# Kernel tuning notes

Measured on AMD Instinct MI355X. Metric: run time of the kernel, lower is better.

The kernel has to match this reference:

```python
import jax, jax.numpy as jnp
import numpy as np

D_MODEL = 768
N_HEADS = 12

def setup_inputs() -> dict:
    key = jax.random.key(0)
    ks = jax.random.split(key, 5)
    D = D_MODEL
    x = jax.random.normal(ks[0], (2, 4096, D), dtype=jnp.float32)
    s_attn = 1.0 / np.sqrt(D)
    s_proj = 1.0 / np.sqrt(D)
    W_attn = jax.random.uniform(ks[1], (D, 3 * D), minval=-s_attn, maxval=s_attn, dtype=jnp.float32)
    b_attn = jax.random.uniform(ks[2], (3 * D,), minval=-s_attn, maxval=s_attn, dtype=jnp.float32)
    W_proj = jax.random.uniform(ks[3], (D, D), minval=-s_proj, maxval=s_proj, dtype=jnp.float32)
    b_proj = jax.random.uniform(ks[4], (D,), minval=-s_proj, maxval=s_proj, dtype=jnp.float32)
    return {"x": x, "W_attn": W_attn, "b_attn": b_attn, "W_proj": W_proj, "b_proj": b_proj}

def reference(x, W_attn, b_attn, W_proj, b_proj):
    B, T, C = x.shape
    H = N_HEADS
    hd = C // H
    qkv = x @ W_attn + b_attn                     # [B,T,3C]
    q, k, v = jnp.split(qkv, 3, axis=-1)
    # [B,T,C] -> [B,H,T,hd]
    q = q.reshape(B, T, H, hd).transpose(0, 2, 1, 3)
    k = k.reshape(B, T, H, hd).transpose(0, 2, 1, 3)
    v = v.reshape(B, T, H, hd).transpose(0, 2, 1, 3)
    att = jnp.einsum('bhqd,bhkd->bhqk', q, k) * (1.0 / np.sqrt(hd))
    causal = jnp.tril(jnp.ones((T, T), dtype=bool))
    att = jnp.where(causal, att, -jnp.inf)
    att = jax.nn.softmax(att, axis=-1)
    y = jnp.einsum('bhqk,bhkd->bhqd', att, v)     # [B,H,T,hd]
    y = y.transpose(0, 2, 1, 3).reshape(B, T, C)
    return y @ W_proj + b_proj
```

## Files before the change

### kernel.cpp

```cpp
#include <hip/hip_runtime.h>
#include <hip/hip_bf16.h>

typedef __attribute__((ext_vector_type(8))) short bf16x8;
typedef __attribute__((ext_vector_type(4))) float f32x4;
typedef __attribute__((ext_vector_type(16))) float f32x16;
typedef __attribute__((ext_vector_type(4))) int i32x4;

#define DEVI __device__ __forceinline__

namespace {
constexpr int BATCH = 2;
constexpr int T = 4096;
constexpr int C = 768;
constexpr int H = 12;
constexpr int HD = 64;
constexpr int M = BATCH * T;
constexpr int N3 = 3 * C;
constexpr int BH = BATCH * H;
constexpr float QSCALE = 0.125f * 1.44269504088896f;
constexpr int PSZ = 64 * 128 + 128;
}

DEVI ushort f2b(float f) {
  union { float f; unsigned u; } v; v.f = f;
  unsigned r = (v.u + 0x7FFFu + ((v.u >> 16) & 1u)) >> 16;
  return (ushort)r;
}

DEVI f32x16 zero16() {
  f32x16 z;
#pragma unroll
  for (int i = 0; i < 16; i++) z[i] = 0.f;
  return z;
}

DEVI void gload16(const void* g, void* l) {
  __builtin_amdgcn_global_load_lds(
      (const __attribute__((address_space(1))) unsigned int*)g,
      (__attribute__((address_space(3))) unsigned int*)l, 16, 0, 0);
}

__global__ __launch_bounds__(256) void cvt_kernel(const float* __restrict__ src,
                                                  ushort* __restrict__ dst, int n) {
  int i = (blockIdx.x * 256 + threadIdx.x) * 4;
  int stride = gridDim.x * 256 * 4;
  for (; i < n; i += stride) {
    float4 v = *reinterpret_cast<const float4*>(src + i);
    ushort4 o;
    o.x = f2b(v.x); o.y = f2b(v.y); o.z = f2b(v.z); o.w = f2b(v.w);
    *reinterpret_cast<ushort4*>(dst + i) = o;
  }
}

__global__ __launch_bounds__(256) void cvtT_kernel(const float* __restrict__ src,
                                                   ushort* __restrict__ dst,
                                                   int K, int N) {
  __shared__ ushort Lt[64 * 68];
  const int k0 = blockIdx.x * 64, n0 = blockIdx.y * 64;
  const int tid = threadIdx.x;
  const int rr = tid >> 4, c4 = (tid & 15) * 4;
#pragma unroll
  for (int it = 0; it < 4; it++) {
    const int r = it * 16 + rr;
    float4 v = *reinterpret_cast<const float4*>(src + (size_t)(k0 + r) * N + n0 + c4);
    Lt[(c4 + 0) * 68 + r] = f2b(v.x);
    Lt[(c4 + 1) * 68 + r] = f2b(v.y);
    Lt[(c4 + 2) * 68 + r] = f2b(v.z);
    Lt[(c4 + 3) * 68 + r] = f2b(v.w);
  }
  __syncthreads();
#pragma unroll
  for (int it = 0; it < 4; it++) {
    const int r = it * 16 + rr;
    *reinterpret_cast<ushort4*>(dst + (size_t)(n0 + r) * K + k0 + c4) =
        *reinterpret_cast<const ushort4*>(&Lt[r * 68 + c4]);
  }
}

template <int EPI>
__global__ __launch_bounds__(256, 3) void gemm_kernel(
    const ushort* __restrict__ A, const ushort* __restrict__ Bt,
    const float* __restrict__ bias, int N, int Kd,
    ushort* __restrict__ qo, ushort* __restrict__ ko, ushort* __restrict__ vo,
    float* __restrict__ fo) {
  constexpr int BM = 128;
  constexpr int BN = 128;
  constexpr int WN = 2;
  constexpr int WTN = BN / WN;
  constexpr int NT = WTN / 32;
  constexpr int CH_A = BM / 8;
  constexpr int CH_B = BN / 8;
  constexpr int CPW = (CH_A + CH_B) / 4;
  constexpr int SMEM = (EPI == 0) ? (4 * 64 * 68) : ((BM + BN) * 64);
  __shared__ ushort smem[SMEM];
  ushort* As = smem;
  ushort* Bs = smem + BM * 64;

  const int tid = threadIdx.x;
  const int lane = tid & 63;
  const int w = tid >> 6;
  const int l31 = lane & 31;
  const int hi = lane >> 5;
  const int wm = w / WN, wn = w % WN;
  const int m0 = blockIdx.y * BM, n0 = blockIdx.x * BN;
  const int r8 = lane >> 3, c8 = lane & 7;
  const int csw = (c8 ^ r8) * 8;

  f32x16 acc[2][NT];
#pragma unroll
  for (int mt = 0; mt < 2; mt++)
#pragma unroll
    for (int nt = 0; nt < NT; nt++) acc[mt][nt] = zero16();

  for (int k0 = 0; k0 < Kd; k0 += 64) {
    __syncthreads();
#pragma unroll
    for (int ci = 0; ci < CPW; ci++) {
      const int chk = w * CPW + ci;
      if (chk < CH_A) {
        gload16(A + (size_t)(m0 + chk * 8 + r8) * Kd + k0 + csw, (char*)As + chk * 1024);
      } else {
        const int ch2 = chk - CH_A;
        gload16(Bt + (size_t)(n0 + ch2 * 8 + r8) * Kd + k0 + csw, (char*)Bs + ch2 * 1024);
      }
    }
    __syncthreads();
#pragma unroll
    for (int ks = 0; ks < 4; ks++) {
      bf16x8 af[2], bf[NT];
#pragma unroll
      for (int mt = 0; mt < 2; mt++) {
        const int rl = wm * 64 + mt * 32 + l31;
        af[mt] = *reinterpret_cast<const bf16x8*>(
            &As[rl * 64 + ((ks * 16 + hi * 8) ^ ((rl & 7) * 8))]);
      }
#pragma unroll
      for (int nt = 0; nt < NT; nt++) {
        const int nl = wn * WTN + nt * 32 + l31;
        bf[nt] = *reinterpret_cast<const bf16x8*>(
            &Bs[nl * 64 + ((ks * 16 + hi * 8) ^ ((nl & 7) * 8))]);
      }
#pragma unroll
      for (int mt = 0; mt < 2; mt++)
#pragma unroll
        for (int nt = 0; nt < NT; nt++)
          acc[mt][nt] = __builtin_amdgcn_mfma_f32_32x32x16_bf16(af[mt], bf[nt], acc[mt][nt], 0, 0, 0);
    }
  }

  if constexpr (EPI == 0) {
    if (n0 >= 1536) {
      __syncthreads();
      ushort* Vw = smem + w * 4352;
      const float bv0 = bias[n0 + wn * 64 + l31];
      const float bv1 = bias[n0 + wn * 64 + 32 + l31];
#pragma unroll
      for (int mt = 0; mt < 2; mt++)
#pragma unroll
        for (int nt = 0; nt < 2; nt++) {
          const float bv = nt ? bv1 : bv0;
#pragma unroll
          for (int r = 0; r < 16; r++) {
            const int trow = mt * 32 + (r & 3) + ((r >> 2) << 3) + (hi << 2);
            Vw[(nt * 32 + l31) * 68 + trow] = f2b(acc[mt][nt][r] + bv);
          }
        }
      const int hh = (n0 - 1536) / 64 + wn;
      const int bb = m0 >> 12;
      const int t0 = (m0 & (T - 1)) + wm * 64;
      const size_t vbase = (size_t)((bb * H + hh) * 64 + lane) * T + t0;
#pragma unroll
      for (int x8 = 0; x8 < 8; x8++) {
        bf16x8 vv = *reinterpret_cast<const bf16x8*>(&Vw[lane * 68 + x8 * 8]);
        *reinterpret_cast<bf16x8*>(vo + vbase + ((x8 ^ (lane & 7)) * 8)) = vv;
      }
    } else {
#pragma unroll
      for (int mt = 0; mt < 2; mt++)
#pragma unroll
        for (int nt = 0; nt < 2; nt++) {
          const int n = n0 + wn * 64 + nt * 32 + l31;
          const float bv = bias[n];
          const int part = (n >= 768) ? 1 : 0;
          const int ci = n - part * 768;
          const int hh = ci >> 6, dd = ci & 63;
#pragma unroll
          for (int r = 0; r < 16; r++) {
            const int m = m0 + wm * 64 + mt * 32 + (r & 3) + ((r >> 2) << 3) + (hi << 2);
            const int bb = m >> 12, t = m & (T - 1);
            const float val = acc[mt][nt][r] + bv;
            if (part == 0) {
              qo[((size_t)(bb * H + hh) * T + t) * HD + dd] = f2b(val * QSCALE);
            } else {
              ko[((size_t)(bb * H + hh) * T + t) * HD + (dd ^ ((t & 7) << 3))] = f2b(val);
            }
          }
        }
    }
  } else {
#pragma unroll
    for (int mt = 0; mt < 2; mt++)
#pragma unroll
      for (int nt = 0; nt < NT; nt++) {
        const int n = n0 + wn * WTN + nt * 32 + l31;
        const float bv = bias[n];
#pragma unroll
        for (int r = 0; r < 16; r++) {
          const int m = m0 + wm * 64 + mt * 32 + (r & 3) + ((r >> 2) << 3) + (hi << 2);
          fo[(size_t)m * N + n] = acc[mt][nt][r] + bv;
        }
      }
  }
}

__global__ __launch_bounds__(256, 3) void attn_kernel(
    const ushort* __restrict__ Qg, const ushort* __restrict__ Kg,
    const ushort* __restrict__ Vtg, ushort* __restrict__ Yg,
    float* __restrict__ Pp) {
  __shared__ ushort kbuf[128 * 64];
  __shared__ ushort vbuf[2 * 2 * 64 * 64];

  const int tid = threadIdx.x;
  const int lane = tid & 63;
  const int w = tid >> 6;
  const int l31 = lane & 31;
  const int hi = lane >> 5;
  const int r8 = lane >> 3, c8 = lane & 7;

  const int bid = blockIdx.x;
  const int xcd = bid & 7, idx = bid >> 3;
  const int bh = xcd * 3 + idx % 3;
  const int slot = idx / 3;

  int qtA, qtB, kvbase, bnd, ntot, pA, pB;
  if (slot < 8) {
    qtA = slot; qtB = 15 - slot; kvbase = 0; bnd = slot + 1; ntot = 17; pA = -1; pB = -1;
  } else if (slot < 24) {
    qtA = slot + 8; qtB = -1; kvbase = 0; bnd = 100; ntot = 16;
    pA = (bh * 16 + (qtA - 16)) * 2; pB = -1;
  } else {
    const int a = slot - 24;
    qtA = 16 + a; qtB = 31 - a; kvbase = 16; bnd = a + 1; ntot = 17;
    pA = (bh * 16 + a) * 2 + 1; pB = (bh * 16 + (15 - a)) * 2 + 1;
  }

  const int bb = bh / H, h = bh % H;
  const ushort* Qp = Qg + (size_t)bh * T * HD;
  const char* Kbp = (const char*)(Kg + (size_t)bh * T * HD);
  const char* Vbp = (const char*)(Vtg + (size_t)bh * HD * T);

  bf16x8 qcur[4];
#pragma unroll
  for (int ks = 0; ks < 4; ks++)
    qcur[ks] = *reinterpret_cast<const bf16x8*>(
        Qp + (size_t)(qtA * 128 + w * 32 + l31) * HD + ks * 16 + hi * 8);

  int q0 = qtA * 128, q0w = q0 + w * 32, qc = q0w + l31;
  int pcur = pA;

  const f32x16 ZF = zero16();
  const i32x4 onesi = {0x3F803F80, 0x3F803F80, 0x3F803F80, 0x3F803F80};
  const bf16x8 onesf = __builtin_bit_cast(bf16x8, onesi);

  f32x16 o16[2];
  o16[0] = zero16();
  o16[1] = zero16();
  f32x16 o_l = zero16();
  const int swz = (l31 & 7) << 3;

  auto issue_K = [&](int kvt) {
    const int kv0 = kvt * 128;
#pragma unroll
    for (int c2 = 0; c2 < 4; c2++) {
      const int chk = w * 4 + c2;
      gload16(Kbp + ((size_t)(kv0 + chk * 8 + r8) * 64 + c8 * 8) * 2,
              (char*)kbuf + chk * 1024);
    }
  };
  auto issue_V = [&](int kvt, int par) {
    const int kv0 = kvt * 128;
#pragma unroll
    for (int c2 = 0; c2 < 4; c2++) {
      const int chk = w * 4 + c2;
      const int st = chk >> 3;
      const int d8 = chk & 7;
      gload16(Vbp + ((size_t)(d8 * 8 + r8) * T + kv0 + st * 64 + c8 * 8) * 2,
              (char*)vbuf + par * 16384 + chk * 1024);
    }
  };

  auto epilogue = [&](int q0p, float lr, ushort* Ytb) {
    ushort* Yw = Ytb + w * 1152;
    const float linv = 1.0f / lr;
#pragma unroll
    for (int dt = 0; dt < 2; dt++) {
#pragma unroll
      for (int r = 0; r < 16; r++) {
        const int d32 = (r & 3) + ((r >> 2) << 3) + (hi << 2);
        Yw[l31 * 36 + d32] = f2b(o16[dt][r] * linv);
      }
#pragma unroll
      for (int seg = 0; seg < 2; seg++) {
        bf16x8 vv = *reinterpret_cast<const bf16x8*>(&Yw[l31 * 36 + hi * 16 + seg * 8]);
        *reinterpret_cast<bf16x8*>(
            Yg + ((size_t)(bb * T + q0p + w * 32 + l31)) * C + h * 64 + dt * 32 +
            hi * 16 + seg * 8) = vv;
      }
    }
  };

  auto pwrite = [&](float* P, float lr) {
#pragma unroll
    for (int dt = 0; dt < 2; dt++)
#pragma unroll
      for (int r = 0; r < 16; r++) {
        const int d = dt * 32 + (r & 3) + ((r >> 2) << 3) + (hi << 2);
        P[d * 128 + w * 32 + l31] = o16[dt][r];
      }
    P[8192 + w * 32 + l31] = lr;
  };

  issue_K(kvbase);
  issue_V(kvbase, 0);

  for (int tt = 0; tt < ntot; tt++) {
    asm volatile("s_waitcnt vmcnt(0)" ::: "memory");
    __builtin_amdgcn_s_barrier();
    __builtin_amdgcn_sched_barrier(0);

    if (tt == bnd) {
      const float lr = o_l[0];
      if (pcur >= 0) pwrite(Pp + (size_t)pcur * PSZ, lr);
      else epilogue(q0, lr, vbuf + ((tt + 1) & 1) * 8192);
      o16[0] = zero16(); o16[1] = zero16(); o_l = zero16();
#pragma unroll
      for (int ks = 0; ks < 4; ks++)
        qcur[ks] = *reinterpret_cast<const bf16x8*>(
            Qp + (size_t)(qtB * 128 + w * 32 + l31) * HD + ks * 16 + hi * 8);
      q0 = qtB * 128; q0w = q0 + w * 32; qc = q0w + l31; pcur = pB;
    }

    const int kvt = kvbase + (tt < bnd ? tt : tt - bnd);
    const int kv0 = kvt * 128;
    bool have[4], needm[4];
#pragma unroll
    for (int sub = 0; sub < 4; sub++) {
      have[sub] = (kv0 + sub * 32) <= (q0w + 31);
      needm[sub] = (kv0 + sub * 32 + 31) > q0w;
    }

    f32x16 s2[4];
#pragma unroll
    for (int sub = 0; sub < 4; sub++) {
      if (!have[sub]) continue;
      const int row = sub * 32 + l31;
      __builtin_amdgcn_s_setprio(1);
      bf16x8 kf = *reinterpret_cast<const bf16x8*>(&kbuf[row * 64 + ((hi * 8) ^ swz)]);
      f32x16 acc = __builtin_amdgcn_mfma_f32_32x32x16_bf16(kf, qcur[0], ZF, 0, 0, 0);
#pragma unroll
      for (int ks = 1; ks < 4; ks++) {
        kf = *reinterpret_cast<const bf16x8*>(
            &kbuf[row * 64 + ((ks * 16 + hi * 8) ^ swz)]);
        acc = __builtin_amdgcn_mfma_f32_32x32x16_bf16(kf, qcur[ks], acc, 0, 0, 0);
      }
      __builtin_amdgcn_s_setprio(0);
      if (needm[sub]) {
#pragma unroll
        for (int r2 = 0; r2 < 16; r2++) {
          const int kv = kv0 + sub * 32 + (r2 & 3) + ((r2 >> 2) << 3) + (hi << 2);
          if (kv > qc) acc[r2] = -1e30f;
        }
      }
      s2[sub] = acc;
    }

    asm volatile("s_waitcnt lgkmcnt(0)" ::: "memory");
    __builtin_amdgcn_s_barrier();
    __builtin_amdgcn_sched_barrier(0);
    if (tt + 1 < ntot) {
      const int nkvt = kvbase + ((tt + 1) < bnd ? (tt + 1) : (tt + 1) - bnd);
      issue_K(nkvt);
      issue_V(nkvt, (tt + 1) & 1);
    }

#pragma unroll
    for (int sub = 0; sub < 4; sub++) {
      if (!have[sub]) continue;
#pragma unroll
      for (int r2 = 0; r2 < 16; r2++)
        s2[sub][r2] = __builtin_amdgcn_exp2f(s2[sub][r2]);
    }

    const ushort* Vpar = vbuf + (tt & 1) * 8192;
#pragma unroll
    for (int sub = 0; sub < 4; sub++) {
      if (!have[sub]) continue;
      const ushort* Vst = Vpar + (sub >> 1) * 4096;
      const int colb = (sub & 1) * 32;
#pragma unroll
      for (int ks2 = 0; ks2 < 2; ks2++) {
        const int r0 = ks2 * 8;
        int a0, a1, b0, b1;
        asm("v_cvt_pk_bf16_f32 %0, %1, %2" : "=v"(a0) : "v"(s2[sub][r0 + 0]), "v"(s2[sub][r0 + 1]));
        asm("v_cvt_pk_bf16_f32 %0, %1, %2" : "=v"(a1) : "v"(s2[sub][r0 + 2]), "v"(s2[sub][r0 + 3]));
        asm("v_cvt_pk_bf16_f32 %0, %1, %2" : "=v"(b0) : "v"(s2[sub][r0 + 4]), "v"(s2[sub][r0 + 5]));
        asm("v_cvt_pk_bf16_f32 %0, %1, %2" : "=v"(b1) : "v"(s2[sub][r0 + 6]), "v"(s2[sub][r0 + 7]));
        asm("v_permlane32_swap_b32 %0, %1" : "+v"(a0), "+v"(b0));
        asm("v_permlane32_swap_b32 %0, %1" : "+v"(a1), "+v"(b1));
        const i32x4 pi = {a0, a1, b0, b1};
        const bf16x8 pf = __builtin_bit_cast(bf16x8, pi);
        __builtin_amdgcn_s_setprio(1);
#pragma unroll
        for (int dt = 0; dt < 2; dt++) {
          const int drow = dt * 32 + l31;
          const int sw2 = (drow & 7) << 3;
          bf16x8 vf = *reinterpret_cast<const bf16x8*>(
              &Vst[drow * 64 + ((colb + ks2 * 16 + hi * 8) ^ sw2)]);
          o16[dt] = __builtin_amdgcn_mfma_f32_32x32x16_bf16(vf, pf, o16[dt], 0, 0, 0);
        }
        o_l = __builtin_amdgcn_mfma_f32_32x32x16_bf16(onesf, pf, o_l, 0, 0, 0);
        __builtin_amdgcn_s_setprio(0);
      }
    }
  }

  {
    const float lr = o_l[0];
    if (pcur >= 0) pwrite(Pp + (size_t)pcur * PSZ, lr);
    else epilogue(q0, lr, vbuf + (ntot & 1) * 8192);
  }
}

__global__ __launch_bounds__(128) void combine_kernel(const float* __restrict__ Pp,
                                                      ushort* __restrict__ Yg) {
  __shared__ ushort Yt[128 * 68];
  const int bid = blockIdx.x;
  const int bh = bid >> 4, qq = bid & 15;
  const int bb = bh / H, h = bh % H;
  const int q0 = (16 + qq) * 128;
  const int q = threadIdx.x;
  const float* P1 = Pp + (size_t)(bh * 16 + qq) * 2 * PSZ;
  const float* P2 = P1 + PSZ;
  const float inv = 1.0f / (P1[8192 + q] + P2[8192 + q]);
#pragma unroll 8
  for (int d = 0; d < 64; d++)
    Yt[q * 68 + d] = f2b((P1[d * 128 + q] + P2[d * 128 + q]) * inv);
  __syncthreads();
#pragma unroll
  for (int it = 0; it < 2; it++) {
    const int row = it * 64 + (q >> 1), half = q & 1;
#pragma unroll
    for (int seg = 0; seg < 4; seg++) {
      bf16x8 vv = *reinterpret_cast<const bf16x8*>(&Yt[row * 68 + half * 32 + seg * 8]);
      *reinterpret_cast<bf16x8*>(
          Yg + ((size_t)(bb * T + q0 + row)) * C + h * 64 + half * 32 + seg * 8) = vv;
    }
  }
}

extern "C" void kernel_launch(void* const* d_in, const int* in_sizes, int n_in,
                              void* d_out, int out_size, void* d_ws, size_t ws_size,
                              hipStream_t stream) {
  const float* x = (const float*)d_in[0];
  const float* Wa = (const float*)d_in[1];
  const float* ba = (const float*)d_in[2];
  const float* Wp = (const float*)d_in[3];
  const float* bp = (const float*)d_in[4];
  float* out = (float*)d_out;

  char* ws = (char*)d_ws;
  size_t off = 0;
  auto carve = [&](size_t bytes) {
    void* p = ws + off;
    off += (bytes + 255) & ~(size_t)255;
    return p;
  };
  ushort* xb   = (ushort*)carve((size_t)M * C * 2);
  ushort* WaT  = (ushort*)carve((size_t)N3 * C * 2);
  ushort* WpT  = (ushort*)carve((size_t)C * C * 2);
  ushort* Qb   = (ushort*)carve((size_t)BH * T * HD * 2);
  ushort* Kb   = (ushort*)carve((size_t)BH * T * HD * 2);
  ushort* Vtb  = (ushort*)carve((size_t)BH * HD * T * 2);
  ushort* Yb   = (ushort*)carve((size_t)M * C * 2);
  float*  Pp   = (float*)carve((size_t)BH * 16 * 2 * PSZ * 4);

  cvt_kernel<<<2048, 256, 0, stream>>>(x, xb, M * C);
  cvtT_kernel<<<dim3(C / 64, N3 / 64), 256, 0, stream>>>(Wa, WaT, C, N3);
  cvtT_kernel<<<dim3(C / 64, C / 64), 256, 0, stream>>>(Wp, WpT, C, C);

  gemm_kernel<0><<<dim3(N3 / 128, M / 128), 256, 0, stream>>>(
      xb, WaT, ba, N3, C, Qb, Kb, Vtb, nullptr);

  attn_kernel<<<dim3(768), 256, 0, stream>>>(Qb, Kb, Vtb, Yb, Pp);
  combine_kernel<<<dim3(BH * 16), 128, 0, stream>>>(Pp, Yb);

  gemm_kernel<1><<<dim3(C / 128, M / 128), 256, 0, stream>>>(
      Yb, WpT, bp, C, C, nullptr, nullptr, nullptr, out);
}
```

Measured before the change: 189.0 us.

## Replace ones-MFMA row-sum with VALU accumulation and rotate KV tile order

The softmax denominator used to come from an extra MFMA against a ones matrix on every PV step. It is now built from four scalar accumulators added alongside the exp2 calls, then combined across the lane halves with a shuffle. Separately, each block now walks its KV tiles in a rotated order based on its block id, to spread concurrent K/V loads across memory. The first part removes a third of the PV-phase MFMAs at the cost of extra VALU adds. The rotation changes which tiles neighbouring blocks read at the same time, but the masked diagonal tile may now run in a different position in the loop.

```diff
diff --git a/kernel.cpp b/kernel.cpp
--- a/kernel.cpp
+++ b/kernel.cpp
@@ -244,6 +244,19 @@
     pA = (bh * 16 + a) * 2 + 1; pB = (bh * 16 + (15 - a)) * 2 + 1;
   }
 
+  const int lenA = (bnd < ntot) ? bnd : ntot;
+  const int lenB = ntot - lenA;
+  const int rotA = (lenA > 1) ? (bid % lenA) : 0;
+  const int rotB = (lenB > 1) ? (bid % lenB) : 0;
+  auto kvt_of = [&](int tt) {
+    if (tt < lenA) {
+      int i = tt + rotA; if (i >= lenA) i -= lenA;
+      return kvbase + i;
+    }
+    int i = (tt - lenA) + rotB; if (i >= lenB) i -= lenB;
+    return kvbase + i;
+  };
+
   const int bb = bh / H, h = bh % H;
   const ushort* Qp = Qg + (size_t)bh * T * HD;
   const char* Kbp = (const char*)(Kg + (size_t)bh * T * HD);
@@ -259,13 +272,11 @@
   int pcur = pA;
 
   const f32x16 ZF = zero16();
-  const i32x4 onesi = {0x3F803F80, 0x3F803F80, 0x3F803F80, 0x3F803F80};
-  const bf16x8 onesf = __builtin_bit_cast(bf16x8, onesi);
 
   f32x16 o16[2];
   o16[0] = zero16();
   o16[1] = zero16();
-  f32x16 o_l = zero16();
+  float sa = 0.f, sb = 0.f, sc = 0.f, sd = 0.f;
   const int swz = (l31 & 7) << 3;
 
   auto issue_K = [&](int kvt) {
@@ -320,8 +331,8 @@
     P[8192 + w * 32 + l31] = lr;
   };
 
-  issue_K(kvbase);
-  issue_V(kvbase, 0);
+  issue_K(kvt_of(0));
+  issue_V(kvt_of(0), 0);
 
   for (int tt = 0; tt < ntot; tt++) {
     asm volatile("s_waitcnt vmcnt(0)" ::: "memory");
@@ -329,10 +340,12 @@
     __builtin_amdgcn_sched_barrier(0);
 
     if (tt == bnd) {
-      const float lr = o_l[0];
+      float lr = (sa + sb) + (sc + sd);
+      lr += __shfl_xor(lr, 32);
       if (pcur >= 0) pwrite(Pp + (size_t)pcur * PSZ, lr);
       else epilogue(q0, lr, vbuf + ((tt + 1) & 1) * 8192);
-      o16[0] = zero16(); o16[1] = zero16(); o_l = zero16();
+      o16[0] = zero16(); o16[1] = zero16();
+      sa = sb = sc = sd = 0.f;
 #pragma unroll
       for (int ks = 0; ks < 4; ks++)
         qcur[ks] = *reinterpret_cast<const bf16x8*>(
@@ -340,7 +353,7 @@
       q0 = qtB * 128; q0w = q0 + w * 32; qc = q0w + l31; pcur = pB;
     }
 
-    const int kvt = kvbase + (tt < bnd ? tt : tt - bnd);
+    const int kvt = kvt_of(tt);
     const int kv0 = kvt * 128;
     bool have[4], needm[4];
 #pragma unroll
@@ -378,7 +391,7 @@
     __builtin_amdgcn_s_barrier();
     __builtin_amdgcn_sched_barrier(0);
     if (tt + 1 < ntot) {
-      const int nkvt = kvbase + ((tt + 1) < bnd ? (tt + 1) : (tt + 1) - bnd);
+      const int nkvt = kvt_of(tt + 1);
       issue_K(nkvt);
       issue_V(nkvt, (tt + 1) & 1);
     }
@@ -387,8 +400,12 @@
     for (int sub = 0; sub < 4; sub++) {
       if (!have[sub]) continue;
 #pragma unroll
-      for (int r2 = 0; r2 < 16; r2++)
-        s2[sub][r2] = __builtin_amdgcn_exp2f(s2[sub][r2]);
+      for (int r2 = 0; r2 < 16; r2 += 4) {
+        s2[sub][r2]     = __builtin_amdgcn_exp2f(s2[sub][r2]);     sa += s2[sub][r2];
+        s2[sub][r2 + 1] = __builtin_amdgcn_exp2f(s2[sub][r2 + 1]); sb += s2[sub][r2 + 1];
+        s2[sub][r2 + 2] = __builtin_amdgcn_exp2f(s2[sub][r2 + 2]); sc += s2[sub][r2 + 2];
+        s2[sub][r2 + 3] = __builtin_amdgcn_exp2f(s2[sub][r2 + 3]); sd += s2[sub][r2 + 3];
+      }
     }
 
     const ushort* Vpar = vbuf + (tt & 1) * 8192;
@@ -418,14 +435,14 @@
               &Vst[drow * 64 + ((colb + ks2 * 16 + hi * 8) ^ sw2)]);
           o16[dt] = __builtin_amdgcn_mfma_f32_32x32x16_bf16(vf, pf, o16[dt], 0, 0, 0);
         }
-        o_l = __builtin_amdgcn_mfma_f32_32x32x16_bf16(onesf, pf, o_l, 0, 0, 0);
         __builtin_amdgcn_s_setprio(0);
       }
     }
   }
 
   {
-    const float lr = o_l[0];
+    float lr = (sa + sb) + (sc + sd);
+    lr += __shfl_xor(lr, 32);
     if (pcur >= 0) pwrite(Pp + (size_t)pcur * PSZ, lr);
     else epilogue(q0, lr, vbuf + (ntot & 1) * 8192);
   }
```

Measured after the change: 176.8 us. 6.4% less time.
